# Performance work log

Hardware: AMD Instinct MI355X
Metric: run time of the kernel (lower is better)

## Reference

```python
import jax, jax.numpy as jnp
import numpy as np

D = 768      # hidden_size
L = 4        # num_hidden_layers
H = 12       # num_attention_heads
I = 3072     # intermediate_size
B, S = 2, 2048
EPS = 1e-5


def setup_inputs() -> dict:
    key = jax.random.key(0)
    ks = jax.random.split(key, 8)
    sc = 0.02
    return {
        "x": jax.random.normal(ks[0], (B, S, D), dtype=jnp.float32),
        # weights stored as [in, out] so y = x @ W + b (same math as torch Linear)
        "qkv_w": jax.random.normal(ks[1], (L, D, 3 * D), dtype=jnp.float32) * sc,
        "qkv_b": jnp.zeros((L, 3 * D), dtype=jnp.float32),
        "out_w": jax.random.normal(ks[2], (L, D, D), dtype=jnp.float32) * sc,
        "out_b": jnp.zeros((L, D), dtype=jnp.float32),
        "ln1_w": jnp.ones((L, D), dtype=jnp.float32),
        "ln1_b": jnp.zeros((L, D), dtype=jnp.float32),
        "fc1_w": jax.random.normal(ks[3], (L, D, I), dtype=jnp.float32) * sc,
        "fc1_b": jnp.zeros((L, I), dtype=jnp.float32),
        "fc2_w": jax.random.normal(ks[4], (L, I, D), dtype=jnp.float32) * sc,
        "fc2_b": jnp.zeros((L, D), dtype=jnp.float32),
        "ln2_w": jnp.ones((L, D), dtype=jnp.float32),
        "ln2_b": jnp.zeros((L, D), dtype=jnp.float32),
    }


def _layer_norm(x, w, b):
    mu = jnp.mean(x, axis=-1, keepdims=True)
    var = jnp.mean(jnp.square(x - mu), axis=-1, keepdims=True)
    return (x - mu) * jax.lax.rsqrt(var + EPS) * w + b


def _encoder(x, qkv_w, qkv_b, out_w, out_b, ln1_w, ln1_b,
             fc1_w, fc1_b, fc2_w, fc2_b, ln2_w, ln2_b):
    hd = D // H
    scale = 1.0 / jnp.sqrt(jnp.float32(hd))

    def block(x, p):
        (qw, qb, ow, ob, l1w, l1b, f1w, f1b, f2w, f2b, l2w, l2b) = p
        # --- attention sub-block (pre-norm residual) ---
        h = _layer_norm(x, l1w, l1b)
        qkv = h @ qw + qb                      # [B,S,3D]
        qkv = qkv.reshape(B, S, H, 3 * hd).transpose(0, 2, 1, 3)  # [B,H,S,3hd]
        q, k, v = jnp.split(qkv, 3, axis=-1)
        logits = jnp.einsum('bhqd,bhkd->bhqk', q, k) * scale       # [B,H,S,S]
        attn = jax.nn.softmax(logits, axis=-1)
        vals = jnp.einsum('bhqk,bhkd->bhqd', attn, v)              # [B,H,S,hd]
        vals = vals.transpose(0, 2, 1, 3).reshape(B, S, D)
        x = x + vals @ ow + ob
        # --- MLP sub-block (pre-norm residual) ---
        h = _layer_norm(x, l2w, l2b)
        h = jax.nn.gelu(h @ f1w + f1b, approximate=False)
        x = x + h @ f2w + f2b
        return x, None

    params = (qkv_w, qkv_b, out_w, out_b, ln1_w, ln1_b,
              fc1_w, fc1_b, fc2_w, fc2_b, ln2_w, ln2_b)
    x, _ = jax.lax.scan(block, x, params)
    return x


def reference(x, qkv_w, qkv_b, out_w, out_b, ln1_w, ln1_b,
              fc1_w, fc1_b, fc2_w, fc2_b, ln2_w, ln2_b):
    return _encoder(x, qkv_w, qkv_b, out_w, out_b, ln1_w, ln1_b,
                    fc1_w, fc1_b, fc2_w, fc2_b, ln2_w, ln2_b)
```

## Files before the change

### kernel.cpp

```cpp
#include <hip/hip_runtime.h>
#include <stdint.h>
#include <math.h>

#define D_MODEL 768
#define NTOK    4096
#define SEQ     2048
#define NHEAD   12
#define HDIM    64
#define D_FF    3072
#define QKV_N   2304

typedef unsigned short ushort_t;
typedef short  sh4    __attribute__((ext_vector_type(4)));
typedef short  short8 __attribute__((ext_vector_type(8)));
typedef float  f32x4  __attribute__((ext_vector_type(4)));

__device__ __forceinline__ float b2f(ushort_t u) {
  union { unsigned int u; float f; } v; v.u = ((unsigned int)u) << 16; return v.f;
}
__device__ __forceinline__ ushort_t f2b(float f) {
  union { float f; unsigned int u; } v; v.f = f;
  unsigned int u = v.u;
  return (ushort_t)((u + 0x7fffu + ((u >> 16) & 1u)) >> 16);
}
__device__ __forceinline__ ushort_t f2b_trunc(float f) {
  union { float f; unsigned int u; } v; v.f = f;
  return (ushort_t)(v.u >> 16);
}

__global__ __launch_bounds__(256) void transpose_layer(
    const float* __restrict__ qkv_w, const float* __restrict__ out_w,
    const float* __restrict__ fc1_w, const float* __restrict__ fc2_w,
    ushort_t* __restrict__ qkvT, ushort_t* __restrict__ outT,
    ushort_t* __restrict__ f1T, ushort_t* __restrict__ f2T) {
  __shared__ ushort_t tile[32][33];
  int bid = blockIdx.x;
  const float* src; ushort_t* dst; int K, N, tn, tk;
  if (bid < 1728)      { src = qkv_w; dst = qkvT; K = 768;  N = 2304; tn = bid % 72;  tk = bid / 72; }
  else if (bid < 2304) { int b = bid - 1728; src = out_w; dst = outT; K = 768;  N = 768;  tn = b % 24; tk = b / 24; }
  else if (bid < 4608) { int b = bid - 2304; src = fc1_w; dst = f1T;  K = 768;  N = 3072; tn = b % 96; tk = b / 96; }
  else                 { int b = bid - 4608; src = fc2_w; dst = f2T;  K = 3072; N = 768;  tn = b % 24; tk = b / 24; }
  int n0 = tn * 32, k0 = tk * 32;
  int tx = threadIdx.x, ty = threadIdx.y;
  #pragma unroll
  for (int i = 0; i < 32; i += 8)
    tile[ty + i][tx] = f2b(src[(size_t)(k0 + ty + i) * N + n0 + tx]);
  __syncthreads();
  #pragma unroll
  for (int i = 0; i < 32; i += 8)
    dst[(size_t)(n0 + ty + i) * K + k0 + tx] = tile[tx][ty + i];
}

__global__ __launch_bounds__(256) void ln_kernel(const float* __restrict__ x,
                                                 const float* __restrict__ w,
                                                 const float* __restrict__ b,
                                                 ushort_t* __restrict__ out) {
  __shared__ float red[4];
  int tok = blockIdx.x, t = threadIdx.x;
  const float* xr = x + (size_t)tok * D_MODEL;
  float v0 = xr[t], v1 = xr[t + 256], v2 = xr[t + 512];
  float s = v0 + v1 + v2;
  #pragma unroll
  for (int o = 1; o < 64; o <<= 1) s += __shfl_xor(s, o, 64);
  if ((t & 63) == 0) red[t >> 6] = s;
  __syncthreads();
  float mean = (red[0] + red[1] + red[2] + red[3]) * (1.0f / 768.0f);
  __syncthreads();
  float d0 = v0 - mean, d1 = v1 - mean, d2 = v2 - mean;
  float q = d0 * d0 + d1 * d1 + d2 * d2;
  #pragma unroll
  for (int o = 1; o < 64; o <<= 1) q += __shfl_xor(q, o, 64);
  if ((t & 63) == 0) red[t >> 6] = q;
  __syncthreads();
  float var = (red[0] + red[1] + red[2] + red[3]) * (1.0f / 768.0f);
  float rs = rsqrtf(var + 1e-5f);
  ushort_t* orow = out + (size_t)tok * D_MODEL;
  orow[t]       = f2b(d0 * rs * w[t]       + b[t]);
  orow[t + 256] = f2b(d1 * rs * w[t + 256] + b[t + 256]);
  orow[t + 512] = f2b(d2 * rs * w[t + 512] + b[t + 512]);
}

template <int EPI, int TN>
__global__ __launch_bounds__(256) void gemm_kernel(
    const ushort_t* __restrict__ A, const ushort_t* __restrict__ BT,
    const float* __restrict__ bias, const float* __restrict__ resid,
    float* __restrict__ Cf, ushort_t* __restrict__ Cb, int M, int N, int K) {
  constexpr int NI = (TN == 128) ? 4 : 2;
  __shared__ ushort_t As[2][128 * 32];
  __shared__ ushort_t Bs[2][TN * 32];
  int t = threadIdx.x;
  int lane = t & 63, wave = t >> 6;
  int m0 = blockIdx.y * 128, n0 = blockIdx.x * TN;
  int wm = (TN == 128) ? (wave & 1) * 64 : wave * 32;
  int wn = (TN == 128) ? (wave >> 1) * 64 : 0;
  int quad = lane >> 4, l16 = lane & 15;
  int kq = quad * 8;
  int lrow = lane >> 2, lcol = (lane & 3) * 8;

  auto stage = [&](int k0, int buf) {
    #pragma unroll
    for (int c = 0; c < 2; ++c) {
      int rowA = wave * 32 + c * 16 + lrow;
      const ushort_t* ga = A + (size_t)(m0 + rowA) * K + k0 + lcol;
      ushort_t* la = &As[buf][(wave * 32 + c * 16) * 32];
      __builtin_amdgcn_global_load_lds((const __attribute__((address_space(1))) void*)ga,
                                       (__attribute__((address_space(3))) void*)la, 16, 0, 0);
      if (TN == 128 || c == 0) {
        int rowB = (TN == 128) ? rowA : (wave * 16 + lrow);
        const ushort_t* gb = BT + (size_t)(n0 + rowB) * K + k0 + lcol;
        ushort_t* lb = (TN == 128) ? &Bs[buf][(wave * 32 + c * 16) * 32]
                                   : &Bs[buf][(wave * 16) * 32];
        __builtin_amdgcn_global_load_lds((const __attribute__((address_space(1))) void*)gb,
                                         (__attribute__((address_space(3))) void*)lb, 16, 0, 0);
      }
    }
  };

  f32x4 acc[NI][4];
  #pragma unroll
  for (int i = 0; i < NI; ++i)
    #pragma unroll
    for (int j = 0; j < 4; ++j) acc[i][j] = (f32x4){0.f, 0.f, 0.f, 0.f};

  stage(0, 0);
  int nk = K / 32;
  for (int ki = 0; ki < nk; ++ki) {
    int cur = ki & 1;
    __syncthreads();
    if (ki + 1 < nk) stage((ki + 1) * 32, cur ^ 1);
    short8 af[NI], bf[4];
    #pragma unroll
    for (int i = 0; i < NI; ++i)
      af[i] = *(const short8*)&As[cur][(wm + i * 16 + l16) * 32 + kq];
    #pragma unroll
    for (int j = 0; j < 4; ++j)
      bf[j] = *(const short8*)&Bs[cur][(wn + j * 16 + l16) * 32 + kq];
    #pragma unroll
    for (int i = 0; i < NI; ++i)
      #pragma unroll
      for (int j = 0; j < 4; ++j)
        acc[i][j] = __builtin_amdgcn_mfma_f32_16x16x32_bf16(af[i], bf[j], acc[i][j], 0, 0, 0);
  }

  #pragma unroll
  for (int i = 0; i < NI; ++i) {
    #pragma unroll
    for (int j = 0; j < 4; ++j) {
      int col = n0 + wn + j * 16 + l16;
      float bv = bias[col];
      #pragma unroll
      for (int r = 0; r < 4; ++r) {
        int row = m0 + wm + i * 16 + quad * 4 + r;
        float v = acc[i][j][r] + bv;
        if (EPI == 1) v = 0.5f * v * (1.0f + erff(v * 0.70710678118654752f));
        if (EPI == 2) v += resid[(size_t)row * N + col];
        if (EPI == 2) Cf[(size_t)row * N + col] = v;
        else          Cb[(size_t)row * N + col] = f2b(v);
      }
    }
  }
}

#define PS_STRIDE 76
__global__ __launch_bounds__(256) void attn_kernel(const ushort_t* __restrict__ qkv,
                                                   ushort_t* __restrict__ out) {
  __shared__ ushort_t Qs[64 * 72];
  __shared__ ushort_t Ks[64 * 72];
  __shared__ ushort_t Vt[64 * 72];
  __shared__ ushort_t Ps[4][16 * PS_STRIDE];
  int t = threadIdx.x;
  int lane = t & 63, wave = t >> 6;
  int quad = lane >> 4, l16 = lane & 15;
  int qt = blockIdx.x;
  int bh = blockIdx.y;
  int b = bh / NHEAD, h = bh % NHEAD;
  size_t base = (size_t)b * SEQ * QKV_N + h * 192;
  int w16 = wave * 16;

  int srow = t >> 2;
  int scol = (t & 3) * 16;
  int vrow = t & 63;
  int vblk = wave * 16;

  {
    const ushort_t* g = qkv + base + (size_t)(qt * 64 + srow) * QKV_N + scol;
    *(short8*)&Qs[srow * 72 + scol]     = *(const short8*)g;
    *(short8*)&Qs[srow * 72 + scol + 8] = *(const short8*)(g + 8);
  }

  float lsum[4];
  f32x4 ofr[4];
  #pragma unroll
  for (int r = 0; r < 4; ++r) lsum[r] = 0.f;
  #pragma unroll
  for (int jd = 0; jd < 4; ++jd) ofr[jd] = (f32x4){0.f, 0.f, 0.f, 0.f};

  const float kscale = 0.125f * 1.44269504088896f;

  for (int kc = 0; kc < SEQ / 64; ++kc) {
    __syncthreads();
    {
      const ushort_t* gk = qkv + base + (size_t)(kc * 64 + srow) * QKV_N + 64 + scol;
      *(short8*)&Ks[srow * 72 + scol]     = *(const short8*)gk;
      *(short8*)&Ks[srow * 72 + scol + 8] = *(const short8*)(gk + 8);
      const ushort_t* gv = qkv + base + (size_t)(kc * 64 + vrow) * QKV_N + 128 + vblk;
      short8 v0 = *(const short8*)gv;
      short8 v1 = *(const short8*)(gv + 8);
      #pragma unroll
      for (int e = 0; e < 8; ++e) {
        Vt[(vblk + e) * 72 + vrow]     = (ushort_t)v0[e];
        Vt[(vblk + 8 + e) * 72 + vrow] = (ushort_t)v1[e];
      }
    }
    __syncthreads();

    f32x4 sfr[4];
    #pragma unroll
    for (int j = 0; j < 4; ++j) sfr[j] = (f32x4){0.f, 0.f, 0.f, 0.f};
    #pragma unroll
    for (int ks = 0; ks < 2; ++ks) {
      short8 aq = *(const short8*)&Qs[(w16 + l16) * 72 + quad * 8 + ks * 32];
      #pragma unroll
      for (int j = 0; j < 4; ++j) {
        short8 bk = *(const short8*)&Ks[(j * 16 + l16) * 72 + quad * 8 + ks * 32];
        sfr[j] = __builtin_amdgcn_mfma_f32_16x16x32_bf16(aq, bk, sfr[j], 0, 0, 0);
      }
    }

    ushort_t* Psw = Ps[wave];
    #pragma unroll
    for (int r = 0; r < 4; ++r) {
      float p0 = exp2f(sfr[0][r] * kscale);
      float p1 = exp2f(sfr[1][r] * kscale);
      float p2 = exp2f(sfr[2][r] * kscale);
      float p3 = exp2f(sfr[3][r] * kscale);
      lsum[r] += (p0 + p1) + (p2 + p3);
      int prow = quad * 4 + r;
      Psw[prow * PS_STRIDE + 0  + l16] = f2b_trunc(p0);
      Psw[prow * PS_STRIDE + 16 + l16] = f2b_trunc(p1);
      Psw[prow * PS_STRIDE + 32 + l16] = f2b_trunc(p2);
      Psw[prow * PS_STRIDE + 48 + l16] = f2b_trunc(p3);
    }

    #pragma unroll
    for (int ks = 0; ks < 2; ++ks) {
      sh4 plo = *(const sh4*)&Psw[l16 * PS_STRIDE + quad * 8 + ks * 32];
      sh4 phi = *(const sh4*)&Psw[l16 * PS_STRIDE + quad * 8 + ks * 32 + 4];
      short8 ap = __builtin_shufflevector(plo, phi, 0, 1, 2, 3, 4, 5, 6, 7);
      #pragma unroll
      for (int jd = 0; jd < 4; ++jd) {
        short8 bv = *(const short8*)&Vt[(jd * 16 + l16) * 72 + quad * 8 + ks * 32];
        ofr[jd] = __builtin_amdgcn_mfma_f32_16x16x32_bf16(ap, bv, ofr[jd], 0, 0, 0);
      }
    }
  }

  #pragma unroll
  for (int r = 0; r < 4; ++r) {
    #pragma unroll
    for (int o = 1; o < 16; o <<= 1) lsum[r] += __shfl_xor(lsum[r], o, 64);
  }

  size_t obase = (size_t)(b * SEQ + qt * 64 + w16) * D_MODEL + h * HDIM;
  #pragma unroll
  for (int r = 0; r < 4; ++r) {
    float inv = 1.0f / lsum[r];
    int row = quad * 4 + r;
    #pragma unroll
    for (int jd = 0; jd < 4; ++jd)
      out[obase + (size_t)row * D_MODEL + jd * 16 + l16] = f2b(ofr[jd][r] * inv);
  }
}

extern "C" void kernel_launch(void* const* d_in, const int* in_sizes, int n_in,
                              void* d_out, int out_size, void* d_ws, size_t ws_size,
                              hipStream_t stream) {
  const float* x_in  = (const float*)d_in[0];
  const float* qkv_w = (const float*)d_in[1];
  const float* qkv_b = (const float*)d_in[2];
  const float* out_w = (const float*)d_in[3];
  const float* out_b = (const float*)d_in[4];
  const float* ln1_w = (const float*)d_in[5];
  const float* ln1_b = (const float*)d_in[6];
  const float* fc1_w = (const float*)d_in[7];
  const float* fc1_b = (const float*)d_in[8];
  const float* fc2_w = (const float*)d_in[9];
  const float* fc2_b = (const float*)d_in[10];
  const float* ln2_w = (const float*)d_in[11];
  const float* ln2_b = (const float*)d_in[12];

  char* ws = (char*)d_ws;
  size_t off = 0;
  auto alloc = [&](size_t bytes) -> void* {
    void* p = ws + off; off += (bytes + 255) & ~(size_t)255; return p;
  };
  float*    buf_x  = (float*)   alloc((size_t)NTOK * D_MODEL * 4);
  float*    buf_x2 = (float*)   alloc((size_t)NTOK * D_MODEL * 4);
  ushort_t* bigb   = (ushort_t*)alloc((size_t)NTOK * D_FF * 2);
  ushort_t* h_b    = (ushort_t*)alloc((size_t)NTOK * D_MODEL * 2);
  ushort_t* at_b   = (ushort_t*)alloc((size_t)NTOK * D_MODEL * 2);
  ushort_t* qkvT   = (ushort_t*)alloc((size_t)QKV_N * D_MODEL * 2);
  ushort_t* outT   = (ushort_t*)alloc((size_t)D_MODEL * D_MODEL * 2);
  ushort_t* f1T    = (ushort_t*)alloc((size_t)D_FF * D_MODEL * 2);
  ushort_t* f2T    = (ushort_t*)alloc((size_t)D_MODEL * D_FF * 2);

  ushort_t* qkv_a = bigb;
  ushort_t* mlp_b = bigb;

  for (int l = 0; l < 4; ++l) {
    const float* resid_in = (l == 0) ? x_in : buf_x;
    transpose_layer<<<6912, dim3(32, 8), 0, stream>>>(
        qkv_w + (size_t)l * D_MODEL * QKV_N, out_w + (size_t)l * D_MODEL * D_MODEL,
        fc1_w + (size_t)l * D_MODEL * D_FF,  fc2_w + (size_t)l * D_FF * D_MODEL,
        qkvT, outT, f1T, f2T);
    ln_kernel<<<NTOK, 256, 0, stream>>>(resid_in, ln1_w + l * D_MODEL, ln1_b + l * D_MODEL, h_b);
    gemm_kernel<0, 128><<<dim3(QKV_N / 128, NTOK / 128), 256, 0, stream>>>(
        h_b, qkvT, qkv_b + l * QKV_N, nullptr, nullptr, qkv_a, NTOK, QKV_N, D_MODEL);
    attn_kernel<<<dim3(SEQ / 64, 2 * NHEAD), 256, 0, stream>>>(qkv_a, at_b);
    gemm_kernel<2, 64><<<dim3(D_MODEL / 64, NTOK / 128), 256, 0, stream>>>(
        at_b, outT, out_b + l * D_MODEL, resid_in, buf_x2, nullptr, NTOK, D_MODEL, D_MODEL);
    ln_kernel<<<NTOK, 256, 0, stream>>>(buf_x2, ln2_w + l * D_MODEL, ln2_b + l * D_MODEL, h_b);
    gemm_kernel<1, 128><<<dim3(D_FF / 128, NTOK / 128), 256, 0, stream>>>(
        h_b, f1T, fc1_b + l * D_FF, nullptr, nullptr, mlp_b, NTOK, D_FF, D_MODEL);
    float* x_next = (l < 3) ? buf_x : (float*)d_out;
    gemm_kernel<2, 64><<<dim3(D_MODEL / 64, NTOK / 128), 256, 0, stream>>>(
        mlp_b, f2T, fc2_b + l * D_MODEL, buf_x2, x_next, nullptr, NTOK, D_MODEL, D_FF);
  }
  (void)in_sizes; (void)n_in; (void)out_size; (void)ws_size;
}
```

Baseline: 1.067 ms.

## Rewrite attention with 32x32 MFMA, register Q, double-buffered K/V and shuffle-based P

The attention kernel now processes 128 query rows per block, with each wave holding 32 query rows in registers instead of staging Q in shared memory. It computes S^T with 32x32x16 bf16 MFMAs and converts P to bf16 with packed cvt instructions. P is rearranged into the A-operand layout with cross-half-wave shuffles rather than a round trip through LDS. K/V tiles are double-buffered, with the next tile's global loads issued before compute, which leaves one barrier per iteration, and setprio is raised around the MFMAs. In exchange it uses more registers and launches half as many blocks, which may reduce occupancy.

```diff
diff --git a/kernel.cpp b/kernel.cpp
--- a/kernel.cpp
+++ b/kernel.cpp
@@ -14,6 +14,7 @@
 typedef short  sh4    __attribute__((ext_vector_type(4)));
 typedef short  short8 __attribute__((ext_vector_type(8)));
 typedef float  f32x4  __attribute__((ext_vector_type(4)));
+typedef float  f32x16 __attribute__((ext_vector_type(16)));
 
 __device__ __forceinline__ float b2f(ushort_t u) {
   union { unsigned int u; float f; } v; v.u = ((unsigned int)u) << 16; return v.f;
@@ -23,9 +24,10 @@
   unsigned int u = v.u;
   return (ushort_t)((u + 0x7fffu + ((u >> 16) & 1u)) >> 16);
 }
-__device__ __forceinline__ ushort_t f2b_trunc(float f) {
-  union { float f; unsigned int u; } v; v.f = f;
-  return (ushort_t)(v.u >> 16);
+__device__ __forceinline__ unsigned cvtpk_bf16(float lo, float hi) {
+  unsigned r;
+  asm("v_cvt_pk_bf16_f32 %0, %1, %2" : "=v"(r) : "v"(lo), "v"(hi));
+  return r;
 }
 
 __global__ __launch_bounds__(256) void transpose_layer(
@@ -161,114 +163,135 @@
   }
 }
 
-#define PS_STRIDE 76
 __global__ __launch_bounds__(256) void attn_kernel(const ushort_t* __restrict__ qkv,
                                                    ushort_t* __restrict__ out) {
-  __shared__ ushort_t Qs[64 * 72];
-  __shared__ ushort_t Ks[64 * 72];
-  __shared__ ushort_t Vt[64 * 72];
-  __shared__ ushort_t Ps[4][16 * PS_STRIDE];
+  __shared__ __align__(16) ushort_t Ks[2][64 * 72];
+  __shared__ __align__(16) ushort_t Vt[2][64 * 72];
   int t = threadIdx.x;
   int lane = t & 63, wave = t >> 6;
-  int quad = lane >> 4, l16 = lane & 15;
+  int l31 = lane & 31, h = lane >> 5, h8 = h * 8;
   int qt = blockIdx.x;
   int bh = blockIdx.y;
-  int b = bh / NHEAD, h = bh % NHEAD;
-  size_t base = (size_t)b * SEQ * QKV_N + h * 192;
-  int w16 = wave * 16;
-
-  int srow = t >> 2;
-  int scol = (t & 3) * 16;
-  int vrow = t & 63;
-  int vblk = wave * 16;
-
+  int b = bh / NHEAD, hd = bh % NHEAD;
+  size_t base = (size_t)b * SEQ * QKV_N + hd * 192;
+
+  const float kscale = 0.125f * 1.44269504088896f;
+
+  short8 qf[4];
   {
-    const ushort_t* g = qkv + base + (size_t)(qt * 64 + srow) * QKV_N + scol;
-    *(short8*)&Qs[srow * 72 + scol]     = *(const short8*)g;
-    *(short8*)&Qs[srow * 72 + scol + 8] = *(const short8*)(g + 8);
-  }
-
-  float lsum[4];
-  f32x4 ofr[4];
-  #pragma unroll
-  for (int r = 0; r < 4; ++r) lsum[r] = 0.f;
-  #pragma unroll
-  for (int jd = 0; jd < 4; ++jd) ofr[jd] = (f32x4){0.f, 0.f, 0.f, 0.f};
-
-  const float kscale = 0.125f * 1.44269504088896f;
-
+    const ushort_t* qp = qkv + base + (size_t)(qt * 128 + wave * 32 + l31) * QKV_N + h8;
+    #pragma unroll
+    for (int ks = 0; ks < 4; ++ks) qf[ks] = *(const short8*)(qp + ks * 16);
+  }
+
+  int srow = t >> 2, scol = (t & 3) * 16;
+  int vrow = t & 63, vblk = wave * 16;
+  short8 kr0, kr1, vr0, vr1;
+  auto kv_load = [&](int kc) {
+    const ushort_t* gk = qkv + base + (size_t)(kc * 64 + srow) * QKV_N + 64 + scol;
+    kr0 = *(const short8*)gk;
+    kr1 = *(const short8*)(gk + 8);
+    const ushort_t* gv = qkv + base + (size_t)(kc * 64 + vrow) * QKV_N + 128 + vblk;
+    vr0 = *(const short8*)gv;
+    vr1 = *(const short8*)(gv + 8);
+  };
+  auto kv_write = [&](int buf) {
+    *(short8*)&Ks[buf][srow * 72 + scol]     = kr0;
+    *(short8*)&Ks[buf][srow * 72 + scol + 8] = kr1;
+    #pragma unroll
+    for (int e = 0; e < 8; ++e) {
+      Vt[buf][(vblk + e) * 72 + vrow]     = (ushort_t)vr0[e];
+      Vt[buf][(vblk + 8 + e) * 72 + vrow] = (ushort_t)vr1[e];
+    }
+  };
+
+  f32x16 o0, o1;
+  #pragma unroll
+  for (int i = 0; i < 16; ++i) { o0[i] = 0.f; o1[i] = 0.f; }
+  float lsum = 0.f;
+
+  kv_load(0);
+  kv_write(0);
+  int cur = 0;
   for (int kc = 0; kc < SEQ / 64; ++kc) {
     __syncthreads();
-    {
-      const ushort_t* gk = qkv + base + (size_t)(kc * 64 + srow) * QKV_N + 64 + scol;
-      *(short8*)&Ks[srow * 72 + scol]     = *(const short8*)gk;
-      *(short8*)&Ks[srow * 72 + scol + 8] = *(const short8*)(gk + 8);
-      const ushort_t* gv = qkv + base + (size_t)(kc * 64 + vrow) * QKV_N + 128 + vblk;
-      short8 v0 = *(const short8*)gv;
-      short8 v1 = *(const short8*)(gv + 8);
+    bool more = (kc + 1 < SEQ / 64);
+    if (more) kv_load(kc + 1);
+
+    f32x16 s0, s1;
+    #pragma unroll
+    for (int i = 0; i < 16; ++i) { s0[i] = 0.f; s1[i] = 0.f; }
+    __builtin_amdgcn_s_setprio(1);
+    #pragma unroll
+    for (int ks = 0; ks < 4; ++ks) {
+      short8 k0 = *(const short8*)&Ks[cur][(l31)      * 72 + ks * 16 + h8];
+      short8 k1 = *(const short8*)&Ks[cur][(32 + l31) * 72 + ks * 16 + h8];
+      s0 = __builtin_amdgcn_mfma_f32_32x32x16_bf16(k0, qf[ks], s0, 0, 0, 0);
+      s1 = __builtin_amdgcn_mfma_f32_32x32x16_bf16(k1, qf[ks], s1, 0, 0, 0);
+    }
+    __builtin_amdgcn_s_setprio(0);
+
+    unsigned wpk[2][4][2];
+    #pragma unroll
+    for (int t2 = 0; t2 < 2; ++t2) {
       #pragma unroll
-      for (int e = 0; e < 8; ++e) {
-        Vt[(vblk + e) * 72 + vrow]     = (ushort_t)v0[e];
-        Vt[(vblk + 8 + e) * 72 + vrow] = (ushort_t)v1[e];
+      for (int g = 0; g < 4; ++g) {
+        float p0, p1, p2, p3;
+        if (t2 == 0) {
+          p0 = exp2f(s0[4 * g + 0] * kscale); p1 = exp2f(s0[4 * g + 1] * kscale);
+          p2 = exp2f(s0[4 * g + 2] * kscale); p3 = exp2f(s0[4 * g + 3] * kscale);
+        } else {
+          p0 = exp2f(s1[4 * g + 0] * kscale); p1 = exp2f(s1[4 * g + 1] * kscale);
+          p2 = exp2f(s1[4 * g + 2] * kscale); p3 = exp2f(s1[4 * g + 3] * kscale);
+        }
+        lsum += (p0 + p1) + (p2 + p3);
+        wpk[t2][g][0] = cvtpk_bf16(p0, p1);
+        wpk[t2][g][1] = cvtpk_bf16(p2, p3);
       }
     }
-    __syncthreads();
-
-    f32x4 sfr[4];
-    #pragma unroll
-    for (int j = 0; j < 4; ++j) sfr[j] = (f32x4){0.f, 0.f, 0.f, 0.f};
-    #pragma unroll
-    for (int ks = 0; ks < 2; ++ks) {
-      short8 aq = *(const short8*)&Qs[(w16 + l16) * 72 + quad * 8 + ks * 32];
+
+    #pragma unroll
+    for (int k4 = 0; k4 < 4; ++k4) {
+      int t2 = k4 >> 1, j2 = (k4 & 1) * 2;
+      unsigned frag[4];
       #pragma unroll
-      for (int j = 0; j < 4; ++j) {
-        short8 bk = *(const short8*)&Ks[(j * 16 + l16) * 72 + quad * 8 + ks * 32];
-        sfr[j] = __builtin_amdgcn_mfma_f32_16x16x32_bf16(aq, bk, sfr[j], 0, 0, 0);
+      for (int c = 0; c < 2; ++c) {
+        unsigned a  = wpk[t2][j2][c];
+        unsigned b2 = wpk[t2][j2 + 1][c];
+        unsigned snd = h ? a : b2;
+        unsigned rcv = (unsigned)__shfl_xor((int)snd, 32, 64);
+        frag[c]     = h ? rcv : a;
+        frag[2 + c] = h ? b2 : rcv;
       }
-    }
-
-    ushort_t* Psw = Ps[wave];
+      union { unsigned u[4]; short8 s8; } uc;
+      uc.u[0] = frag[0]; uc.u[1] = frag[1]; uc.u[2] = frag[2]; uc.u[3] = frag[3];
+      short8 ap = uc.s8;
+      short8 v0 = *(const short8*)&Vt[cur][(l31)      * 72 + k4 * 16 + h8];
+      short8 v1 = *(const short8*)&Vt[cur][(32 + l31) * 72 + k4 * 16 + h8];
+      __builtin_amdgcn_s_setprio(1);
+      o0 = __builtin_amdgcn_mfma_f32_32x32x16_bf16(ap, v0, o0, 0, 0, 0);
+      o1 = __builtin_amdgcn_mfma_f32_32x32x16_bf16(ap, v1, o1, 0, 0, 0);
+      __builtin_amdgcn_s_setprio(0);
+    }
+
+    if (more) kv_write(cur ^ 1);
+    cur ^= 1;
+  }
+
+  lsum += __shfl_xor(lsum, 32, 64);
+
+  size_t obase = (size_t)(b * SEQ + qt * 128 + wave * 32) * D_MODEL + hd * HDIM;
+  #pragma unroll
+  for (int g = 0; g < 4; ++g) {
     #pragma unroll
     for (int r = 0; r < 4; ++r) {
-      float p0 = exp2f(sfr[0][r] * kscale);
-      float p1 = exp2f(sfr[1][r] * kscale);
-      float p2 = exp2f(sfr[2][r] * kscale);
-      float p3 = exp2f(sfr[3][r] * kscale);
-      lsum[r] += (p0 + p1) + (p2 + p3);
-      int prow = quad * 4 + r;
-      Psw[prow * PS_STRIDE + 0  + l16] = f2b_trunc(p0);
-      Psw[prow * PS_STRIDE + 16 + l16] = f2b_trunc(p1);
-      Psw[prow * PS_STRIDE + 32 + l16] = f2b_trunc(p2);
-      Psw[prow * PS_STRIDE + 48 + l16] = f2b_trunc(p3);
-    }
-
-    #pragma unroll
-    for (int ks = 0; ks < 2; ++ks) {
-      sh4 plo = *(const sh4*)&Psw[l16 * PS_STRIDE + quad * 8 + ks * 32];
-      sh4 phi = *(const sh4*)&Psw[l16 * PS_STRIDE + quad * 8 + ks * 32 + 4];
-      short8 ap = __builtin_shufflevector(plo, phi, 0, 1, 2, 3, 4, 5, 6, 7);
-      #pragma unroll
-      for (int jd = 0; jd < 4; ++jd) {
-        short8 bv = *(const short8*)&Vt[(jd * 16 + l16) * 72 + quad * 8 + ks * 32];
-        ofr[jd] = __builtin_amdgcn_mfma_f32_16x16x32_bf16(ap, bv, ofr[jd], 0, 0, 0);
-      }
-    }
-  }
-
-  #pragma unroll
-  for (int r = 0; r < 4; ++r) {
-    #pragma unroll
-    for (int o = 1; o < 16; o <<= 1) lsum[r] += __shfl_xor(lsum[r], o, 64);
-  }
-
-  size_t obase = (size_t)(b * SEQ + qt * 64 + w16) * D_MODEL + h * HDIM;
-  #pragma unroll
-  for (int r = 0; r < 4; ++r) {
-    float inv = 1.0f / lsum[r];
-    int row = quad * 4 + r;
-    #pragma unroll
-    for (int jd = 0; jd < 4; ++jd)
-      out[obase + (size_t)row * D_MODEL + jd * 16 + l16] = f2b(ofr[jd][r] * inv);
+      int reg = 4 * g + r;
+      int qrow = r + 8 * g + 4 * h;
+      float inv = 1.0f / __shfl(lsum, qrow, 64);
+      ushort_t* orow = out + obase + (size_t)qrow * D_MODEL;
+      orow[l31]      = f2b(o0[reg] * inv);
+      orow[32 + l31] = f2b(o1[reg] * inv);
+    }
   }
 }
 
@@ -316,7 +339,7 @@
     ln_kernel<<<NTOK, 256, 0, stream>>>(resid_in, ln1_w + l * D_MODEL, ln1_b + l * D_MODEL, h_b);
     gemm_kernel<0, 128><<<dim3(QKV_N / 128, NTOK / 128), 256, 0, stream>>>(
         h_b, qkvT, qkv_b + l * QKV_N, nullptr, nullptr, qkv_a, NTOK, QKV_N, D_MODEL);
-    attn_kernel<<<dim3(SEQ / 64, 2 * NHEAD), 256, 0, stream>>>(qkv_a, at_b);
+    attn_kernel<<<dim3(SEQ / 128, 2 * NHEAD), 256, 0, stream>>>(qkv_a, at_b);
     gemm_kernel<2, 64><<<dim3(D_MODEL / 64, NTOK / 128), 256, 0, stream>>>(
         at_b, outT, out_b + l * D_MODEL, resid_in, buf_x2, nullptr, NTOK, D_MODEL, D_MODEL);
     ln_kernel<<<NTOK, 256, 0, stream>>>(buf_x2, ln2_w + l * D_MODEL, ln2_b + l * D_MODEL, h_b);
```

New measurement: 1.048 ms. Within noise of the previous version (-1.8%).
